# Optimization experiments

Hardware: AMD Instinct MI355X
Metric: run time of the kernel (lower is better)

## Reference

```python
import jax, jax.numpy as jnp
import numpy as np

N_NODES = 50000
N_EDGES = 640000
D = 128
N_GRAPHS = 64
N_CLASSES = 32
N_LAYERS = 4


def setup_inputs() -> dict:
    key = jax.random.key(0)
    ks = jax.random.split(key, 8)
    x = jax.random.normal(ks[0], (N_NODES, D), dtype=jnp.float32)
    edge_index = jax.random.randint(ks[1], (2, N_EDGES), 0, N_NODES, dtype=jnp.int64)
    batch = jnp.sort(jax.random.randint(ks[2], (N_NODES,), 0, N_GRAPHS, dtype=jnp.int64))
    s = 0.05  # small init scale (stand-in for init_weights)
    w1 = jax.random.normal(ks[3], (N_LAYERS, D, D), dtype=jnp.float32) * s
    b1 = jnp.zeros((N_LAYERS, D), dtype=jnp.float32)
    w2 = jax.random.normal(ks[4], (N_LAYERS, D, D), dtype=jnp.float32) * s
    b2 = jnp.zeros((N_LAYERS, D), dtype=jnp.float32)
    w_lin = jax.random.normal(ks[5], (D, N_CLASSES), dtype=jnp.float32) * s
    b_lin = jnp.zeros((N_CLASSES,), dtype=jnp.float32)
    return {"x": x, "edge_index": edge_index, "batch": batch,
            "w1": w1, "b1": b1, "w2": w2, "b2": b2,
            "w_lin": w_lin, "b_lin": b_lin}


def reference(x, edge_index, batch, w1, b1, w2, b2, w_lin, b_lin):
    # GIN stack: num_layers GINConv layers (eps=0, sum aggregation,
    # MLP = Linear -> ReLU -> Linear), ReLU between layers (not after last).
    src, dst = edge_index[0], edge_index[1]
    n = x.shape[0]
    h = x
    for i in range(N_LAYERS):
        # neighbor sum aggregation: scatter-add messages h[src] into dst
        agg = jax.ops.segment_sum(h[src], dst, num_segments=n)
        z = h + agg  # (1 + eps) * x_i + sum_j x_j, eps = 0
        z = jnp.maximum(z @ w1[i] + b1[i], 0.0)
        h = z @ w2[i] + b2[i]
        if i < N_LAYERS - 1:
            h = jax.nn.relu(h)
    # global_mean_pool over graph ids
    sums = jax.ops.segment_sum(h, batch, num_segments=N_GRAPHS)
    counts = jax.ops.segment_sum(jnp.ones((n,), dtype=h.dtype), batch, num_segments=N_GRAPHS)
    pooled = sums / jnp.maximum(counts, 1.0)[:, None]
    logits = pooled @ w_lin + b_lin
    return (pooled, logits)
```

## Files before the change

### kernel.cpp

```cpp
#include <hip/hip_runtime.h>
#include <hip/hip_fp16.h>


typedef short short8 __attribute__((ext_vector_type(8)));
typedef float floatx4 __attribute__((ext_vector_type(4)));

#define TM 32
#define ZSTRIDE 136
#define CSTRIDE 16

__device__ __forceinline__ unsigned short f2bf(float x) {
    unsigned int u = __float_as_uint(x);
    u += 0x7fffu + ((u >> 16) & 1u);
    return (unsigned short)(u >> 16);
}
__device__ __forceinline__ float bf2f(unsigned short h) {
    return __uint_as_float(((unsigned int)h) << 16);
}

__device__ __forceinline__ float2 ldrowh(const char* __restrict__ base,
                                         int id, unsigned laneoff) {
    __half2 h = *(const __half2*)(base + ((unsigned)id << 8) + laneoff);
    return __half22float2(h);
}


__global__ __launch_bounds__(256) void gin_build1(
    const int* __restrict__ dst, int nEdges, int* __restrict__ counts,
    int* __restrict__ rank,
    const float* __restrict__ w1, const float* __restrict__ w2,
    unsigned short* __restrict__ whf, unsigned short* __restrict__ wlf, int wTotal,
    const float* __restrict__ x, __half* __restrict__ xh, int nNodes) {
    const int gsize = gridDim.x * 256;
    const int gtid = blockIdx.x * 256 + threadIdx.x;
    for (int idx = gtid; idx < wTotal; idx += gsize) {
        int mat  = idx >> 14;
        int rem  = idx & 16383;
        int kc   = rem >> 12;
        int ct   = (rem >> 9) & 7;
        int lane = (rem >> 3) & 63;
        int j    = rem & 7;
        int row = kc * 32 + (lane >> 4) * 8 + j;
        int col = ct * 16 + (lane & 15);
        int L = mat >> 1;
        const float* W = (mat & 1) ? (w2 + (size_t)L * 16384) : (w1 + (size_t)L * 16384);
        float v = W[row * 128 + col];
        unsigned short h = f2bf(v);
        unsigned short l = f2bf(v - bf2f(h));
        whf[idx] = h;
        wlf[idx] = l;
    }
    const int total4 = nNodes * 32;
    for (int i = gtid; i < total4; i += gsize) {
        float4 v = ((const float4*)x)[i];
        union { __half2 h[2]; float2 f; } u;
        u.h[0] = __halves2half2(__float2half_rn(v.x), __float2half_rn(v.y));
        u.h[1] = __halves2half2(__float2half_rn(v.z), __float2half_rn(v.w));
        ((float2*)xh)[i] = u.f;
    }
    for (int i = gtid; i < nEdges; i += gsize)
        rank[i] = atomicAdd(&counts[(size_t)dst[i] * CSTRIDE], 1);
}


__global__ __launch_bounds__(256) void gin_scanA(const int* __restrict__ counts,
                                                 int* __restrict__ offsLocal,
                                                 int* __restrict__ partials, int n) {
    __shared__ int s[256];
    int t = threadIdx.x;
    int i = blockIdx.x * 256 + t;
    int v = (i < n) ? counts[(size_t)i * CSTRIDE] : 0;
    s[t] = v;
    __syncthreads();
    for (int off = 1; off < 256; off <<= 1) {
        int u = (t >= off) ? s[t - off] : 0;
        __syncthreads();
        s[t] += u;
        __syncthreads();
    }
    if (i < n) offsLocal[i] = s[t] - v;
    if (t == 255) partials[blockIdx.x] = s[255];
}


__global__ __launch_bounds__(256) void gin_scatfuse(
    const int* __restrict__ src, const int* __restrict__ dst,
    const int* __restrict__ rank, int nEdges,
    const int* __restrict__ offsLocal, const int* __restrict__ partials,
    int nb, int* __restrict__ offsFinal, int* __restrict__ ssrc, int nNodes) {
    __shared__ int s[256];
    __shared__ int base[256];
    int t = threadIdx.x;
    s[t] = (t < nb) ? partials[t] : 0;
    __syncthreads();
    for (int off = 1; off < 256; off <<= 1) {
        int u = (t >= off) ? s[t - off] : 0;
        __syncthreads();
        s[t] += u;
        __syncthreads();
    }
    base[t] = (t > 0) ? s[t - 1] : 0;
    __syncthreads();

    int i = blockIdx.x * 256 + t;
    if (i < nEdges) {
        int d = dst[i];
        int p = offsLocal[d] + base[d >> 8] + rank[i];
        ssrc[p] = src[i];
    }
    if (blockIdx.x < (unsigned)nb) {
        int j = blockIdx.x * 256 + t;
        if (j < nNodes) offsFinal[j] = offsLocal[j] + base[blockIdx.x];
        if (j == 0) offsFinal[nNodes] = nEdges;
    }
}


__global__ __launch_bounds__(256) void gin_layer(const __half* __restrict__ hin,
                                                 const int* __restrict__ offs,
                                                 const int* __restrict__ ssrc,
                                                 const unsigned short* __restrict__ whf,
                                                 const unsigned short* __restrict__ wlf,
                                                 int matBase,
                                                 const float* __restrict__ b1p,
                                                 const float* __restrict__ b2p,
                                                 __half* __restrict__ hout,
                                                 const int* __restrict__ batch,
                                                 float* __restrict__ gsums,
                                                 int nNodes, int lastLayer) {
    __shared__ unsigned short smem[2 * TM * ZSTRIDE];
    unsigned short* zh = smem;
    unsigned short* zl = smem + TM * ZSTRIDE;
    const int tid = threadIdx.x;
    const int w = tid >> 6, lane = tid & 63;
    const int lo4 = lane & 15, hi4 = lane >> 4;
    const int rowbase = blockIdx.x * TM;
    const char* hbase = (const char*)hin;
    const unsigned laneoff = (unsigned)lane * 4u;

    const int gbase = rowbase + w * 8;
#pragma unroll
    for (int pp = 0; pp < 4; ++pp) {
        int nA = gbase + 2 * pp, nB = nA + 1;
        bool okA = nA < nNodes, okB = nB < nNodes;
        float2 aA = make_float2(0.f, 0.f), aB = make_float2(0.f, 0.f);
        if (okA) aA = ldrowh(hbase, nA, laneoff);
        if (okB) aB = ldrowh(hbase, nB, laneoff);
        int eA = okA ? offs[nA] : 0, endA = okA ? offs[nA + 1] : 0;
        int eB = okB ? offs[nB] : 0, endB = okB ? offs[nB + 1] : 0;

        while (eA + 4 <= endA && eB + 4 <= endB) {
            int sA0 = ssrc[eA], sA1 = ssrc[eA + 1], sA2 = ssrc[eA + 2], sA3 = ssrc[eA + 3];
            int sB0 = ssrc[eB], sB1 = ssrc[eB + 1], sB2 = ssrc[eB + 2], sB3 = ssrc[eB + 3];
            float2 vA0 = ldrowh(hbase, sA0, laneoff);
            float2 vA1 = ldrowh(hbase, sA1, laneoff);
            float2 vA2 = ldrowh(hbase, sA2, laneoff);
            float2 vA3 = ldrowh(hbase, sA3, laneoff);
            float2 vB0 = ldrowh(hbase, sB0, laneoff);
            float2 vB1 = ldrowh(hbase, sB1, laneoff);
            float2 vB2 = ldrowh(hbase, sB2, laneoff);
            float2 vB3 = ldrowh(hbase, sB3, laneoff);
            aA.x += (vA0.x + vA1.x) + (vA2.x + vA3.x);
            aA.y += (vA0.y + vA1.y) + (vA2.y + vA3.y);
            aB.x += (vB0.x + vB1.x) + (vB2.x + vB3.x);
            aB.y += (vB0.y + vB1.y) + (vB2.y + vB3.y);
            eA += 4; eB += 4;
        }
        for (; eA + 4 <= endA; eA += 4) {
            int s0 = ssrc[eA], s1 = ssrc[eA + 1], s2 = ssrc[eA + 2], s3 = ssrc[eA + 3];
            float2 v0 = ldrowh(hbase, s0, laneoff);
            float2 v1 = ldrowh(hbase, s1, laneoff);
            float2 v2 = ldrowh(hbase, s2, laneoff);
            float2 v3 = ldrowh(hbase, s3, laneoff);
            aA.x += (v0.x + v1.x) + (v2.x + v3.x);
            aA.y += (v0.y + v1.y) + (v2.y + v3.y);
        }
        for (; eA < endA; ++eA) {
            float2 v = ldrowh(hbase, ssrc[eA], laneoff);
            aA.x += v.x; aA.y += v.y;
        }
        for (; eB + 4 <= endB; eB += 4) {
            int s0 = ssrc[eB], s1 = ssrc[eB + 1], s2 = ssrc[eB + 2], s3 = ssrc[eB + 3];
            float2 v0 = ldrowh(hbase, s0, laneoff);
            float2 v1 = ldrowh(hbase, s1, laneoff);
            float2 v2 = ldrowh(hbase, s2, laneoff);
            float2 v3 = ldrowh(hbase, s3, laneoff);
            aB.x += (v0.x + v1.x) + (v2.x + v3.x);
            aB.y += (v0.y + v1.y) + (v2.y + v3.y);
        }
        for (; eB < endB; ++eB) {
            float2 v = ldrowh(hbase, ssrc[eB], laneoff);
            aB.x += v.x; aB.y += v.y;
        }
        int rA = nA - rowbase, rB = rA + 1;
        unsigned short hx = f2bf(aA.x), hy = f2bf(aA.y);
        ((unsigned int*)zh)[rA * (ZSTRIDE / 2) + lane] = (unsigned)hx | ((unsigned)hy << 16);
        ((unsigned int*)zl)[rA * (ZSTRIDE / 2) + lane] =
            (unsigned)f2bf(aA.x - bf2f(hx)) | ((unsigned)f2bf(aA.y - bf2f(hy)) << 16);
        hx = f2bf(aB.x); hy = f2bf(aB.y);
        ((unsigned int*)zh)[rB * (ZSTRIDE / 2) + lane] = (unsigned)hx | ((unsigned)hy << 16);
        ((unsigned int*)zl)[rB * (ZSTRIDE / 2) + lane] =
            (unsigned)f2bf(aB.x - bf2f(hx)) | ((unsigned)f2bf(aB.y - bf2f(hy)) << 16);
    }
    __syncthreads();

    floatx4 acc[2][2];
#pragma unroll
    for (int rg = 0; rg < 2; ++rg)
#pragma unroll
        for (int ct = 0; ct < 2; ++ct) acc[rg][ct] = (floatx4)0.f;

    for (int kc = 0; kc < 4; ++kc) {
        size_t o0 = ((((size_t)matBase * 4 + kc) * 8 + (2 * w)) * 64 + lane) * 8;
        size_t o1 = ((((size_t)matBase * 4 + kc) * 8 + (2 * w + 1)) * 64 + lane) * 8;
        short8 bh0 = *(const short8*)(whf + o0), bl0 = *(const short8*)(wlf + o0);
        short8 bh1 = *(const short8*)(whf + o1), bl1 = *(const short8*)(wlf + o1);
#pragma unroll
        for (int rg = 0; rg < 2; ++rg) {
            const int rbase = (rg * 16 + lo4) * ZSTRIDE + kc * 32 + hi4 * 8;
            short8 ah = *(const short8*)(zh + rbase);
            short8 al = *(const short8*)(zl + rbase);
            acc[rg][0] = __builtin_amdgcn_mfma_f32_16x16x32_bf16(ah, bh0, acc[rg][0], 0, 0, 0);
            acc[rg][0] = __builtin_amdgcn_mfma_f32_16x16x32_bf16(al, bh0, acc[rg][0], 0, 0, 0);
            acc[rg][0] = __builtin_amdgcn_mfma_f32_16x16x32_bf16(ah, bl0, acc[rg][0], 0, 0, 0);
            acc[rg][1] = __builtin_amdgcn_mfma_f32_16x16x32_bf16(ah, bh1, acc[rg][1], 0, 0, 0);
            acc[rg][1] = __builtin_amdgcn_mfma_f32_16x16x32_bf16(al, bh1, acc[rg][1], 0, 0, 0);
            acc[rg][1] = __builtin_amdgcn_mfma_f32_16x16x32_bf16(ah, bl1, acc[rg][1], 0, 0, 0);
        }
    }
    __syncthreads();

    float bb1_0 = b1p[w * 32 + lo4];
    float bb1_1 = b1p[w * 32 + 16 + lo4];
#pragma unroll
    for (int rg = 0; rg < 2; ++rg)
#pragma unroll
        for (int ct = 0; ct < 2; ++ct) {
            float bb = ct ? bb1_1 : bb1_0;
#pragma unroll
            for (int r = 0; r < 4; ++r) {
                float v = fmaxf(acc[rg][ct][r] + bb, 0.f);
                unsigned short h = f2bf(v);
                int idx = (rg * 16 + hi4 * 4 + r) * ZSTRIDE + w * 32 + ct * 16 + lo4;
                zh[idx] = h;
                zl[idx] = f2bf(v - bf2f(h));
            }
        }
    __syncthreads();

#pragma unroll
    for (int rg = 0; rg < 2; ++rg)
#pragma unroll
        for (int ct = 0; ct < 2; ++ct) acc[rg][ct] = (floatx4)0.f;

    for (int kc = 0; kc < 4; ++kc) {
        size_t o0 = ((((size_t)(matBase + 1) * 4 + kc) * 8 + (2 * w)) * 64 + lane) * 8;
        size_t o1 = ((((size_t)(matBase + 1) * 4 + kc) * 8 + (2 * w + 1)) * 64 + lane) * 8;
        short8 bh0 = *(const short8*)(whf + o0), bl0 = *(const short8*)(wlf + o0);
        short8 bh1 = *(const short8*)(whf + o1), bl1 = *(const short8*)(wlf + o1);
#pragma unroll
        for (int rg = 0; rg < 2; ++rg) {
            const int rbase = (rg * 16 + lo4) * ZSTRIDE + kc * 32 + hi4 * 8;
            short8 ah = *(const short8*)(zh + rbase);
            short8 al = *(const short8*)(zl + rbase);
            acc[rg][0] = __builtin_amdgcn_mfma_f32_16x16x32_bf16(ah, bh0, acc[rg][0], 0, 0, 0);
            acc[rg][0] = __builtin_amdgcn_mfma_f32_16x16x32_bf16(al, bh0, acc[rg][0], 0, 0, 0);
            acc[rg][0] = __builtin_amdgcn_mfma_f32_16x16x32_bf16(ah, bl0, acc[rg][0], 0, 0, 0);
            acc[rg][1] = __builtin_amdgcn_mfma_f32_16x16x32_bf16(ah, bh1, acc[rg][1], 0, 0, 0);
            acc[rg][1] = __builtin_amdgcn_mfma_f32_16x16x32_bf16(al, bh1, acc[rg][1], 0, 0, 0);
            acc[rg][1] = __builtin_amdgcn_mfma_f32_16x16x32_bf16(ah, bl1, acc[rg][1], 0, 0, 0);
        }
    }

    float bb2_0 = b2p[w * 32 + lo4];
    float bb2_1 = b2p[w * 32 + 16 + lo4];

    if (!lastLayer) {
#pragma unroll
        for (int rg = 0; rg < 2; ++rg)
#pragma unroll
            for (int ct = 0; ct < 2; ++ct) {
                float bb = ct ? bb2_1 : bb2_0;
#pragma unroll
                for (int r = 0; r < 4; ++r) {
                    int row = rowbase + rg * 16 + hi4 * 4 + r;
                    if (row < nNodes) {
                        float v = fmaxf(acc[rg][ct][r] + bb, 0.f);
                        hout[(size_t)row * 128 + w * 32 + ct * 16 + lo4] = __float2half_rn(v);
                    }
                }
            }
    } else {
        __syncthreads();
        float* zf = (float*)smem;
#pragma unroll
        for (int rg = 0; rg < 2; ++rg)
#pragma unroll
            for (int ct = 0; ct < 2; ++ct) {
                float bb = ct ? bb2_1 : bb2_0;
#pragma unroll
                for (int r = 0; r < 4; ++r)
                    zf[(rg * 16 + hi4 * 4 + r) * 132 + w * 32 + ct * 16 + lo4] =
                        acc[rg][ct][r] + bb;
            }
        __syncthreads();
        int c = tid & 127, half = tid >> 7;
        int rmax = nNodes - rowbase;
        if (rmax > TM) rmax = TM;
        float accp = 0.f;
        int gcur = -1;
        for (int r = half; r < rmax; r += 2) {
            int g = batch[rowbase + r];
            if (g != gcur) {
                if (gcur >= 0) atomicAdd(&gsums[gcur * 128 + c], accp);
                accp = 0.f;
                gcur = g;
            }
            accp += zf[r * 132 + c];
        }
        if (gcur >= 0) atomicAdd(&gsums[gcur * 128 + c], accp);
    }
}


__device__ __forceinline__ int lb_search(const int* __restrict__ a, int n, int key) {
    int lo = 0, hi = n;
    while (lo < hi) {
        int m = (lo + hi) >> 1;
        if (a[m] < key) lo = m + 1; else hi = m;
    }
    return lo;
}

__global__ __launch_bounds__(128) void gin_pool2(const float* __restrict__ gsums,
                                                 const int* __restrict__ batch, int nNodes,
                                                 const float* __restrict__ wlin,
                                                 const float* __restrict__ blin,
                                                 float* __restrict__ out, int nGraphs) {
    __shared__ float sp[128];
    int g = blockIdx.x;
    int t = threadIdx.x;
    int start = lb_search(batch, nNodes, g);
    int end   = lb_search(batch, nNodes, g + 1);
    float cnt = (float)(end - start);
    float p = gsums[(size_t)g * 128 + t] / fmaxf(cnt, 1.0f);
    out[(size_t)g * 128 + t] = p;
    sp[t] = p;
    __syncthreads();
    if (t < 32) {
        float s = blin[t];
        for (int k = 0; k < 128; ++k) s += sp[k] * wlin[k * 32 + t];
        out[(size_t)nGraphs * 128 + g * 32 + t] = s;
    }
}


extern "C" void kernel_launch(void* const* d_in, const int* in_sizes, int n_in,
                              void* d_out, int out_size, void* d_ws, size_t ws_size,
                              hipStream_t stream) {
    const float* x     = (const float*)d_in[0];
    const int*   ei    = (const int*)d_in[1];
    const int*   batch = (const int*)d_in[2];
    const float* w1    = (const float*)d_in[3];
    const float* b1    = (const float*)d_in[4];
    const float* w2    = (const float*)d_in[5];
    const float* b2    = (const float*)d_in[6];
    const float* wlin  = (const float*)d_in[7];
    const float* blin  = (const float*)d_in[8];
    float* out = (float*)d_out;

    const int nNodes  = in_sizes[0] / 128;
    const int nEdges  = in_sizes[1] / 2;
    const int nLayers = in_sizes[3] / (128 * 128);
    const int nGraphs = out_size / 160;

    const int* srcArr = ei;
    const int* dstArr = ei + nEdges;

    char* p = (char*)d_ws;
    int*   counts    = (int*)p;           p += (size_t)nNodes * CSTRIDE * 4;
    float* gsums     = (float*)p;         p += (size_t)nGraphs * 128 * 4;
    int*   offsLocal = (int*)p;           p += (size_t)(nNodes + 1) * 4;
    int*   offsFinal = (int*)p;           p += (size_t)(nNodes + 1) * 4;
    int*   rank      = (int*)p;           p += (size_t)nEdges * 4;
    int*   partials  = (int*)p;           p += 256 * 4;
    int*   ssrc      = (int*)p;           p += (size_t)nEdges * 4;

    p = (char*)(((uintptr_t)p + 63) & ~(uintptr_t)63);
    const int wTotal = nLayers * 2 * 16384;
    unsigned short* whf = (unsigned short*)p;  p += (size_t)wTotal * 2;
    unsigned short* wlf = (unsigned short*)p;  p += (size_t)wTotal * 2;

    p = (char*)(((uintptr_t)p + 63) & ~(uintptr_t)63);
    __half* xh   = (__half*)p;            p += (size_t)nNodes * 128 * 2;
    __half* bufA = (__half*)p;            p += (size_t)nNodes * 128 * 2;
    __half* bufB = (__half*)p;

    const size_t zeroBytes = ((size_t)nNodes * CSTRIDE + (size_t)nGraphs * 128) * 4;
    hipMemsetAsync(d_ws, 0, zeroBytes, stream);

    const int eb = (nEdges + 255) / 256;
    const int nb = (nNodes + 255) / 256;

    gin_build1<<<eb, 256, 0, stream>>>(dstArr, nEdges, counts, rank, w1, w2,
                                       whf, wlf, wTotal, x, xh, nNodes);
    gin_scanA<<<nb, 256, 0, stream>>>(counts, offsLocal, partials, nNodes);
    gin_scatfuse<<<eb, 256, 0, stream>>>(srcArr, dstArr, rank, nEdges,
                                         offsLocal, partials, nb,
                                         offsFinal, ssrc, nNodes);

    const int lb = (nNodes + TM - 1) / TM;
    const __half* hin = xh;
    __half* bufs[2] = {bufA, bufB};
    for (int L = 0; L < nLayers; ++L) {
        int last = (L == nLayers - 1);
        __half* hout = bufs[L & 1];
        gin_layer<<<lb, 256, 0, stream>>>(hin, offsFinal, ssrc, whf, wlf, 2 * L,
                                          b1 + (size_t)L * 128, b2 + (size_t)L * 128,
                                          hout, batch, gsums, nNodes, last);
        hin = hout;
    }
    gin_pool2<<<nGraphs, 128, 0, stream>>>(gsums, batch, nNodes, wlin, blin, out, nGraphs);
}
```

Measured before the change: 312.7 us.

## Fuse pooling/classifier into last layer via last-block counter; unpad degree counts

Removes the separate pooling kernel. The last GIN layer now increments a global done-counter, and the final block to finish computes the graph counts, the mean-pooled features and the logits. Separately, the per-node degree counters are no longer padded to 16 ints each, which shrinks the memset and makes the counters denser. The denser counters risk more atomic contention on shared cache lines, and the tail work becomes serial in a single block.

```diff
diff --git a/kernel.cpp b/kernel.cpp
--- a/kernel.cpp
+++ b/kernel.cpp
@@ -7,7 +7,6 @@
 
 #define TM 32
 #define ZSTRIDE 136
-#define CSTRIDE 16
 
 __device__ __forceinline__ unsigned short f2bf(float x) {
     unsigned int u = __float_as_uint(x);
@@ -22,6 +21,15 @@
                                          int id, unsigned laneoff) {
     __half2 h = *(const __half2*)(base + ((unsigned)id << 8) + laneoff);
     return __half22float2(h);
+}
+
+__device__ __forceinline__ int lb_search(const int* __restrict__ a, int n, int key) {
+    int lo = 0, hi = n;
+    while (lo < hi) {
+        int m = (lo + hi) >> 1;
+        if (a[m] < key) lo = m + 1; else hi = m;
+    }
+    return lo;
 }
 
 
@@ -59,7 +67,7 @@
         ((float2*)xh)[i] = u.f;
     }
     for (int i = gtid; i < nEdges; i += gsize)
-        rank[i] = atomicAdd(&counts[(size_t)dst[i] * CSTRIDE], 1);
+        rank[i] = atomicAdd(&counts[dst[i]], 1);
 }
 
 
@@ -69,7 +77,7 @@
     __shared__ int s[256];
     int t = threadIdx.x;
     int i = blockIdx.x * 256 + t;
-    int v = (i < n) ? counts[(size_t)i * CSTRIDE] : 0;
+    int v = (i < n) ? counts[i] : 0;
     s[t] = v;
     __syncthreads();
     for (int off = 1; off < 256; off <<= 1) {
@@ -127,8 +135,15 @@
                                                  __half* __restrict__ hout,
                                                  const int* __restrict__ batch,
                                                  float* __restrict__ gsums,
+                                                 int* __restrict__ donecnt,
+                                                 const float* __restrict__ wlin,
+                                                 const float* __restrict__ blin,
+                                                 float* __restrict__ out,
+                                                 int nGraphs,
                                                  int nNodes, int lastLayer) {
     __shared__ unsigned short smem[2 * TM * ZSTRIDE];
+    __shared__ float cntS[128];
+    __shared__ int amLast;
     unsigned short* zh = smem;
     unsigned short* zl = smem + TM * ZSTRIDE;
     const int tid = threadIdx.x;
@@ -319,38 +334,34 @@
             accp += zf[r * 132 + c];
         }
         if (gcur >= 0) atomicAdd(&gsums[gcur * 128 + c], accp);
-    }
-}
-
-
-__device__ __forceinline__ int lb_search(const int* __restrict__ a, int n, int key) {
-    int lo = 0, hi = n;
-    while (lo < hi) {
-        int m = (lo + hi) >> 1;
-        if (a[m] < key) lo = m + 1; else hi = m;
-    }
-    return lo;
-}
-
-__global__ __launch_bounds__(128) void gin_pool2(const float* __restrict__ gsums,
-                                                 const int* __restrict__ batch, int nNodes,
-                                                 const float* __restrict__ wlin,
-                                                 const float* __restrict__ blin,
-                                                 float* __restrict__ out, int nGraphs) {
-    __shared__ float sp[128];
-    int g = blockIdx.x;
-    int t = threadIdx.x;
-    int start = lb_search(batch, nNodes, g);
-    int end   = lb_search(batch, nNodes, g + 1);
-    float cnt = (float)(end - start);
-    float p = gsums[(size_t)g * 128 + t] / fmaxf(cnt, 1.0f);
-    out[(size_t)g * 128 + t] = p;
-    sp[t] = p;
-    __syncthreads();
-    if (t < 32) {
-        float s = blin[t];
-        for (int k = 0; k < 128; ++k) s += sp[k] * wlin[k * 32 + t];
-        out[(size_t)nGraphs * 128 + g * 32 + t] = s;
+
+        __threadfence();
+        if (tid == 0)
+            amLast = (atomicAdd(donecnt, 1) == (int)gridDim.x - 1);
+        __syncthreads();
+        if (amLast) {
+            __threadfence();
+            for (int g = tid; g < nGraphs; g += 256) {
+                int s = lb_search(batch, nNodes, g);
+                int e = lb_search(batch, nNodes, g + 1);
+                cntS[g] = fmaxf((float)(e - s), 1.0f);
+            }
+            __syncthreads();
+            const int np = nGraphs * 128;
+            for (int i = tid; i < np; i += 256) {
+                int g = i >> 7, cc = i & 127;
+                out[(size_t)g * 128 + cc] = gsums[(size_t)g * 128 + cc] / cntS[g];
+            }
+            __syncthreads();
+            const int nl = nGraphs * 32;
+            for (int i = tid; i < nl; i += 256) {
+                int g = i >> 5, kk = i & 31;
+                float s = blin[kk];
+                const float* po = out + (size_t)g * 128;
+                for (int cc = 0; cc < 128; ++cc) s += po[cc] * wlin[cc * 32 + kk];
+                out[(size_t)nGraphs * 128 + g * 32 + kk] = s;
+            }
+        }
     }
 }
 
@@ -378,8 +389,9 @@
     const int* dstArr = ei + nEdges;
 
     char* p = (char*)d_ws;
-    int*   counts    = (int*)p;           p += (size_t)nNodes * CSTRIDE * 4;
+    int*   counts    = (int*)p;           p += (size_t)nNodes * 4;
     float* gsums     = (float*)p;         p += (size_t)nGraphs * 128 * 4;
+    int*   donecnt   = (int*)p;           p += 4;
     int*   offsLocal = (int*)p;           p += (size_t)(nNodes + 1) * 4;
     int*   offsFinal = (int*)p;           p += (size_t)(nNodes + 1) * 4;
     int*   rank      = (int*)p;           p += (size_t)nEdges * 4;
@@ -396,7 +408,7 @@
     __half* bufA = (__half*)p;            p += (size_t)nNodes * 128 * 2;
     __half* bufB = (__half*)p;
 
-    const size_t zeroBytes = ((size_t)nNodes * CSTRIDE + (size_t)nGraphs * 128) * 4;
+    const size_t zeroBytes = ((size_t)nNodes + (size_t)nGraphs * 128 + 1) * 4;
     hipMemsetAsync(d_ws, 0, zeroBytes, stream);
 
     const int eb = (nEdges + 255) / 256;
@@ -417,8 +429,9 @@
         __half* hout = bufs[L & 1];
         gin_layer<<<lb, 256, 0, stream>>>(hin, offsFinal, ssrc, whf, wlf, 2 * L,
                                           b1 + (size_t)L * 128, b2 + (size_t)L * 128,
-                                          hout, batch, gsums, nNodes, last);
+                                          hout, batch, gsums, donecnt,
+                                          wlin, blin, out, nGraphs,
+                                          nNodes, last);
         hin = hout;
     }
-    gin_pool2<<<nGraphs, 128, 0, stream>>>(gsums, batch, nNodes, wlin, blin, out, nGraphs);
-}
+}
```

Result: slower. 500.4 us (+60.0%).
